# Kernel tuning notes

Hardware: AMD Instinct MI355X
Metric: run time of the kernel (lower is better)

The kernel has to match this reference:

```python
import jax, jax.numpy as jnp
import numpy as np

B, C_IN, C_OUT, N, K = 1, 64, 64, 50000, 20


def setup_inputs() -> dict:
    key = jax.random.key(0)
    k1, k2, k3, k4, k5 = jax.random.split(key, 5)
    x = jax.random.normal(k1, (B, C_IN, N, 1), dtype=jnp.float32)
    edge_index = jax.random.randint(k2, (2, B, N, K), 0, N, dtype=jnp.int64)
    dis = jax.random.uniform(k3, (B, N, K), dtype=jnp.float32)
    W = jax.random.normal(k4, (C_OUT, 2 * C_IN), dtype=jnp.float32) * (2.0 / (2 * C_IN)) ** 0.5
    b = jnp.zeros((C_OUT,), dtype=jnp.float32)
    att_w = jax.random.normal(k5, (K,), dtype=jnp.float32) * (2.0 / K) ** 0.5
    att_b = jnp.zeros((1,), dtype=jnp.float32)
    return {"x": x, "edge_index": edge_index, "dis": dis, "W": W, "b": b,
            "att_w": att_w, "att_b": att_b}


def reference(x, edge_index, dis, W, b, att_w, att_b):
    # x: [B, C, N, 1]; edge_index: [2, B, N, K]; dis: [B, N, K]
    x2 = x[..., 0]  # [B, C, N]
    gather = jax.vmap(lambda xb, ib: xb[:, ib])  # per-batch: [C,N] idx[N,K] -> [C,N,K]
    x_i = gather(x2, edge_index[1])  # [B, C, N, K]
    x_j = gather(x2, edge_index[0])  # [B, C, N, K]
    feat = jnp.concatenate([x_i, x_j - x_i], axis=1)  # [B, 2C, N, K]
    # 1x1 conv == channel contraction
    feat = jax.nn.relu(jnp.einsum('oc,bcnk->bonk', W, feat) + b[None, :, None, None])
    # attention over the k channel of dis -> per-node scaler
    scaler = jnp.tanh(jnp.einsum('k,bnk->bn', att_w, dis) + att_b) + 1.0  # [B, N]
    suppression = 2.0 * jax.nn.sigmoid(-dis * scaler[:, :, None])  # [B, N, K]
    feat = feat * suppression[:, None, :, :]  # [B, C_out, N, K]
    return jnp.max(feat, axis=-1, keepdims=True)  # [B, C_out, N, 1]
```

## Files before the change

kernel.cpp:

```cpp
#include <hip/hip_runtime.h>
#include <hip/hip_bf16.h>

#define NN 50000
#define CC 64
#define KK 20

static __device__ __forceinline__ ushort f2bf(float f) {
    unsigned int u = __float_as_uint(f);
    unsigned int r = (u + 0x7FFFu + ((u >> 16) & 1u)) >> 16;
    return (ushort)r;
}
static __device__ __forceinline__ float bf2f(ushort v) {
    return __uint_as_float(((unsigned int)v) << 16);
}

__global__ __launch_bounds__(256) void prep_kernel(
    const float* __restrict__ x,
    const float* __restrict__ W,
    const float* __restrict__ b,
    ushort* __restrict__ yA,
    ushort* __restrict__ yB)
{
    __shared__ float At[64][65];
    __shared__ float Bt[64][65];
    __shared__ float xt[64][68];

    const int t = threadIdx.x;
    for (int i = t; i < 64 * 64; i += 256) {
        int c = i >> 6, ci = i & 63;
        float w1 = W[c * 128 + ci];
        float w2 = W[c * 128 + 64 + ci];
        At[ci][c] = w1 - w2;
        Bt[ci][c] = w2;
    }

    const int n0 = blockIdx.x * 64;
    const int g  = t >> 6;
    const int nl = t & 63;
    #pragma unroll
    for (int i = 0; i < 16; i++) {
        int ci = i * 4 + g;
        int nn = n0 + nl;
        xt[ci][nl] = (nn < NN) ? x[ci * NN + nn] : 0.f;
    }
    __syncthreads();

    const int c = t & 63;
    float accA[16], accB[16];
    #pragma unroll
    for (int j = 0; j < 16; j++) { accA[j] = 0.f; accB[j] = 0.f; }

    for (int ci = 0; ci < 64; ci++) {
        float a  = At[ci][c];
        float w2 = Bt[ci][c];
        const float4* xr = reinterpret_cast<const float4*>(&xt[ci][g * 16]);
        #pragma unroll
        for (int q = 0; q < 4; q++) {
            float4 xv = xr[q];
            accA[q * 4 + 0] += a * xv.x;  accB[q * 4 + 0] += w2 * xv.x;
            accA[q * 4 + 1] += a * xv.y;  accB[q * 4 + 1] += w2 * xv.y;
            accA[q * 4 + 2] += a * xv.z;  accB[q * 4 + 2] += w2 * xv.z;
            accA[q * 4 + 3] += a * xv.w;  accB[q * 4 + 3] += w2 * xv.w;
        }
    }

    float bias = b[c];
    #pragma unroll
    for (int j = 0; j < 16; j++) {
        int n = n0 + g * 16 + j;
        if (n < NN) {
            yA[n * 64 + c] = f2bf(accA[j] + bias);
            yB[n * 64 + c] = f2bf(accB[j]);
        }
    }
}

__global__ __launch_bounds__(256) void edge_kernel(
    const ushort* __restrict__ yA,
    const ushort* __restrict__ yB,
    const int* __restrict__ ej,
    const int* __restrict__ ei,
    const float* __restrict__ dis,
    const float* __restrict__ att_w,
    const float* __restrict__ att_b,
    float* __restrict__ out)
{
    __shared__ float tile[16][65];

    const int t    = threadIdx.x;
    const int lane = t & 63;
    const int w    = t >> 6;
    const int n0   = blockIdx.x * 16;

    const float aw = (lane < KK) ? att_w[lane] : 0.f;
    const float ab = att_b[0];

    #pragma unroll
    for (int s = 0; s < 4; s++) {
        const int nl = w * 4 + s;
        const int n  = n0 + nl;

        float d = 0.f; int ii = 0, jj = 0;
        if (lane < KK) {
            d  = dis[n * KK + lane];
            ii = ei[n * KK + lane];
            jj = ej[n * KK + lane];
        }
        float p = aw * d;
        #pragma unroll
        for (int off = 16; off > 0; off >>= 1) p += __shfl_down(p, off);
        const float scaler = tanhf(__shfl(p, 0) + ab) + 1.0f;
        const float sup = 2.0f / (1.0f + __expf(d * scaler));

        float m = 0.f;
        #pragma unroll
        for (int k = 0; k < KK; k++) {
            const int   i_k = __shfl(ii, k);
            const int   j_k = __shfl(jj, k);
            const float s_k = __shfl(sup, k);
            float a = bf2f(yA[(size_t)i_k * 64 + lane]);
            float bv = bf2f(yB[(size_t)j_k * 64 + lane]);
            float v = fmaxf(a + bv, 0.f);
            m = fmaxf(m, v * s_k);
        }
        tile[nl][lane] = m;
    }
    __syncthreads();

    #pragma unroll
    for (int it = 0; it < 4; it++) {
        const int c  = it * 16 + (t >> 4);
        const int nl = t & 15;
        out[(size_t)c * NN + n0 + nl] = tile[nl][c];
    }
}

extern "C" void kernel_launch(void* const* d_in, const int* in_sizes, int n_in,
                              void* d_out, int out_size, void* d_ws, size_t ws_size,
                              hipStream_t stream) {
    const float* x     = (const float*)d_in[0];
    const int*   e     = (const int*)d_in[1];
    const float* dis   = (const float*)d_in[2];
    const float* W     = (const float*)d_in[3];
    const float* b     = (const float*)d_in[4];
    const float* att_w = (const float*)d_in[5];
    const float* att_b = (const float*)d_in[6];
    float* out = (float*)d_out;

    ushort* yA = (ushort*)d_ws;
    ushort* yB = yA + (size_t)NN * 64;

    prep_kernel<<<(NN + 63) / 64, 256, 0, stream>>>(x, W, b, yA, yB);
    edge_kernel<<<NN / 16, 256, 0, stream>>>(yA, yB, e, e + NN * KK, dis,
                                             att_w, att_b, out);
}
```

Baseline: 143.9 us.

## Vectorize edge gathers to 4 channels per lane and batch neighbor loads

The edge kernel now has each lane load 8 bytes (4 bf16 channels) per gathered row, so one wavefront covers 4 neighbors per iteration. It reduces the per-neighbor max across the 4 lane groups with xor shuffles, which cuts the gather loop from 20 iterations to 5. Index, distance and suppression values for all 4 nodes are loaded up front to expose more memory-level parallelism. In exchange it adds cross-lane reductions and register pressure.

```diff
diff --git a/kernel.cpp b/kernel.cpp
--- a/kernel.cpp
+++ b/kernel.cpp
@@ -10,8 +10,11 @@
     unsigned int r = (u + 0x7FFFu + ((u >> 16) & 1u)) >> 16;
     return (ushort)r;
 }
-static __device__ __forceinline__ float bf2f(ushort v) {
-    return __uint_as_float(((unsigned int)v) << 16);
+static __device__ __forceinline__ float bfl(unsigned int u) {
+    return __uint_as_float(u << 16);
+}
+static __device__ __forceinline__ float bfh(unsigned int u) {
+    return __uint_as_float(u & 0xffff0000u);
 }
 
 __global__ __launch_bounds__(256) void prep_kernel(
@@ -85,45 +88,70 @@
     const float* __restrict__ att_b,
     float* __restrict__ out)
 {
-    __shared__ float tile[16][65];
+    __shared__ float tile[16][68];
 
     const int t    = threadIdx.x;
     const int lane = t & 63;
     const int w    = t >> 6;
+    const int g    = lane >> 4;
+    const int l    = lane & 15;
     const int n0   = blockIdx.x * 16;
+    const int nb   = n0 + w * 4;
 
     const float aw = (lane < KK) ? att_w[lane] : 0.f;
     const float ab = att_b[0];
 
+    float d4[4]; int ii4[4], jj4[4];
     #pragma unroll
     for (int s = 0; s < 4; s++) {
-        const int nl = w * 4 + s;
-        const int n  = n0 + nl;
-
+        const int n = nb + s;
         float d = 0.f; int ii = 0, jj = 0;
         if (lane < KK) {
             d  = dis[n * KK + lane];
             ii = ei[n * KK + lane];
             jj = ej[n * KK + lane];
         }
-        float p = aw * d;
+        d4[s] = d; ii4[s] = ii; jj4[s] = jj;
+    }
+
+    float sup4[4];
+    #pragma unroll
+    for (int s = 0; s < 4; s++) {
+        float p = aw * d4[s];
         #pragma unroll
         for (int off = 16; off > 0; off >>= 1) p += __shfl_down(p, off);
         const float scaler = tanhf(__shfl(p, 0) + ab) + 1.0f;
-        const float sup = 2.0f / (1.0f + __expf(d * scaler));
+        sup4[s] = 2.0f / (1.0f + __expf(d4[s] * scaler));
+    }
 
-        float m = 0.f;
+    const uint2* A2 = (const uint2*)yA;
+    const uint2* B2 = (const uint2*)yB;
+
+    #pragma unroll
+    for (int s = 0; s < 4; s++) {
+        float4 m = {0.f, 0.f, 0.f, 0.f};
         #pragma unroll
-        for (int k = 0; k < KK; k++) {
-            const int   i_k = __shfl(ii, k);
-            const int   j_k = __shfl(jj, k);
-            const float s_k = __shfl(sup, k);
-            float a = bf2f(yA[(size_t)i_k * 64 + lane]);
-            float bv = bf2f(yB[(size_t)j_k * 64 + lane]);
-            float v = fmaxf(a + bv, 0.f);
-            m = fmaxf(m, v * s_k);
+        for (int kb = 0; kb < 5; kb++) {
+            const int   src = kb * 4 + g;
+            const int   i_k = __shfl(ii4[s], src);
+            const int   j_k = __shfl(jj4[s], src);
+            const float sp  = __shfl(sup4[s], src);
+            const uint2 a = A2[(size_t)i_k * 16 + l];
+            const uint2 bb = B2[(size_t)j_k * 16 + l];
+            float v;
+            v = fmaxf(bfl(a.x) + bfl(bb.x), 0.f) * sp;  m.x = fmaxf(m.x, v);
+            v = fmaxf(bfh(a.x) + bfh(bb.x), 0.f) * sp;  m.y = fmaxf(m.y, v);
+            v = fmaxf(bfl(a.y) + bfl(bb.y), 0.f) * sp;  m.z = fmaxf(m.z, v);
+            v = fmaxf(bfh(a.y) + bfh(bb.y), 0.f) * sp;  m.w = fmaxf(m.w, v);
         }
-        tile[nl][lane] = m;
+        #pragma unroll
+        for (int mask = 16; mask <= 32; mask <<= 1) {
+            m.x = fmaxf(m.x, __shfl_xor(m.x, mask));
+            m.y = fmaxf(m.y, __shfl_xor(m.y, mask));
+            m.z = fmaxf(m.z, __shfl_xor(m.z, mask));
+            m.w = fmaxf(m.w, __shfl_xor(m.w, mask));
+        }
+        if (g == 0) *(float4*)&tile[w * 4 + s][l * 4] = m;
     }
     __syncthreads();
 
```

After: 133.8 us. 1.08x faster.
